# Performance work log

Measured on AMD Instinct MI355X. Metric: run time of the kernel, lower is better.

## Reference

```python
import jax, jax.numpy as jnp
import numpy as np

N, E, F_IN, D, EF, L, G = 50000, 800000, 92, 64, 50, 3, 128
EPS = 1e-5


def setup_inputs() -> dict:
    key = jax.random.key(0)
    ks = jax.random.split(key, 16)
    Z = 2 * D + EF  # concat dim for CGConv messages
    inp = {
        "x": jax.random.normal(ks[0], (N, F_IN), dtype=jnp.float32),
        "edge_index": jax.random.randint(ks[1], (2, E), 0, N, dtype=jnp.int32),
        "edge_attr": jax.random.uniform(ks[2], (E, EF), dtype=jnp.float32),
        "batch": jnp.sort(jax.random.randint(ks[3], (N,), 0, G, dtype=jnp.int32)),
        "pre_W": jax.random.normal(ks[4], (F_IN, D), dtype=jnp.float32) * 0.05,
        "pre_b": jnp.zeros((D,), jnp.float32),
        "Wf": jax.random.normal(ks[5], (L, Z, D), dtype=jnp.float32) * 0.05,
        "bf": jnp.zeros((L, D), jnp.float32),
        "Ws": jax.random.normal(ks[6], (L, Z, D), dtype=jnp.float32) * 0.05,
        "bs": jnp.zeros((L, D), jnp.float32),
        "bn_gamma": jnp.ones((L, D), jnp.float32) + 0.1 * jax.random.normal(ks[7], (L, D), dtype=jnp.float32),
        "bn_beta": 0.1 * jax.random.normal(ks[8], (L, D), dtype=jnp.float32),
        "bn_mean": 0.1 * jax.random.normal(ks[9], (L, D), dtype=jnp.float32),
        "bn_var": jax.random.uniform(ks[10], (L, D), dtype=jnp.float32, minval=0.5, maxval=1.5),
        "post_W": jax.random.normal(ks[11], (D, D), dtype=jnp.float32) * 0.05,
        "post_b": jnp.zeros((D,), jnp.float32),
        "out_W": jax.random.normal(ks[12], (D, 1), dtype=jnp.float32) * 0.05,
        "out_b": jnp.zeros((1,), jnp.float32),
    }
    return inp


def reference(x, edge_index, edge_attr, batch, pre_W, pre_b, Wf, bf, Ws, bs,
              bn_gamma, bn_beta, bn_mean, bn_var, post_W, post_b, out_W, out_b):
    src = edge_index[0]  # x_j (source)
    dst = edge_index[1]  # x_i (target, aggregation index)

    # pre FC + relu
    h = jax.nn.relu(x @ pre_W + pre_b)

    # in-degree for mean aggregation
    deg = jax.ops.segment_sum(jnp.ones((E,), h.dtype), dst, num_segments=N)
    deg = jnp.maximum(deg, 1.0)[:, None]

    for l in range(L):
        # CGConv: z_ij = [h_i || h_j || e_ij]
        z = jnp.concatenate([h[dst], h[src], edge_attr], axis=-1)  # [E, 2D+EF]
        m = jax.nn.sigmoid(z @ Wf[l] + bf[l]) * jax.nn.softplus(z @ Ws[l] + bs[l])
        agg = jax.ops.segment_sum(m, dst, num_segments=N) / deg
        h = h + agg  # residual in CGConv
        # BatchNorm1d (eval mode, running stats); dropout is identity in eval
        h = bn_gamma[l] * (h - bn_mean[l]) * jax.lax.rsqrt(bn_var[l] + EPS) + bn_beta[l]

    # early global_mean_pool over graphs
    cnt = jax.ops.segment_sum(jnp.ones((N,), h.dtype), batch, num_segments=G)
    cnt = jnp.maximum(cnt, 1.0)[:, None]
    g = jax.ops.segment_sum(h, batch, num_segments=G) / cnt  # [G, D]

    g = jax.nn.relu(g @ post_W + post_b)
    return g @ out_W + out_b  # [G, 1]
```

## Files before the change

### kernel.cpp

```cpp
#include <hip/hip_runtime.h>
#include <cmath>

#define N_NODES 50000
#define N_EDGES 800000
#define F_IN 92
#define DIM 64
#define EF 50
#define NLAYER 3
#define NGRAPH 128
#define ZROWS 178

__global__ __launch_bounds__(256, 3) void pre_fc(const float* __restrict__ x,
                                                 const float* __restrict__ W,
                                                 const float* __restrict__ b,
                                                 float* __restrict__ h, int N)
{
    const int lane = threadIdx.x & 63;
    const int wid  = blockIdx.x * (blockDim.x >> 6) + (threadIdx.x >> 6);
    const int nw   = gridDim.x * (blockDim.x >> 6);
    float w[F_IN];
#pragma unroll
    for (int k = 0; k < F_IN; ++k) w[k] = W[k * DIM + lane];
    const float bb = b[lane];
#pragma unroll 1
    for (int n = wid; n < N; n += nw) {
        const int nu = __builtin_amdgcn_readfirstlane(n);
        const float* xr = x + (size_t)nu * F_IN;
        float a = bb;
#pragma unroll
        for (int k = 0; k < F_IN; ++k) a = fmaf(xr[k], w[k], a);
        h[(size_t)nu * DIM + lane] = fmaxf(a, 0.f);
    }
}

__global__ __launch_bounds__(256) void hist_cnt(const int* __restrict__ ei, int E,
                                                const int* __restrict__ batch, int N,
                                                int* __restrict__ hist,
                                                float* __restrict__ cnt)
{
    const int i = blockIdx.x * blockDim.x + threadIdx.x;
    const int stride = gridDim.x * blockDim.x;
    for (int e = i; e < E; e += stride) atomicAdd(&hist[ei[E + e]], 1);
    for (int n = i; n < N; n += stride) unsafeAtomicAdd(&cnt[batch[n]], 1.f);
}

__global__ __launch_bounds__(256) void scan_offs(const int* __restrict__ hist,
                                                 int* __restrict__ offs, int Nn)
{
    __shared__ int ssum[256];
    const int t = threadIdx.x;
    const int seg = (Nn + 255) / 256;
    const int lo = t * seg;
    const int hi = (lo + seg < Nn) ? lo + seg : Nn;
    int s = 0;
    for (int i = lo; i < hi; ++i) s += hist[i];
    ssum[t] = s;
    __syncthreads();
    if (t == 0) {
        int run = 0;
        for (int i = 0; i < 256; ++i) { int v = ssum[i]; ssum[i] = run; run += v; }
        offs[Nn] = run;
    }
    __syncthreads();
    int run = ssum[t];
    for (int i = lo; i < hi; ++i) { offs[i] = run; run += hist[i]; }
}

__global__ __launch_bounds__(256) void scatter_edges(const int* __restrict__ ei,
                                                     const int* __restrict__ offs,
                                                     int* __restrict__ cursor,
                                                     int* __restrict__ s_src,
                                                     int* __restrict__ s_dst,
                                                     int* __restrict__ s_eid, int E)
{
    const int i = blockIdx.x * blockDim.x + threadIdx.x;
    const int stride = gridDim.x * blockDim.x;
    for (int e = i; e < E; e += stride) {
        const int d = ei[E + e];
        const int s = ei[e];
        const int pos = offs[d] + atomicAdd(&cursor[d], 1);
        s_src[pos] = s;
        s_dst[pos] = d;
        s_eid[pos] = e;
    }
}

__global__ __launch_bounds__(256, 2) void node_proj(const float* __restrict__ h,
                                                    const float* __restrict__ Wfl,
                                                    const float* __restrict__ Wsl,
                                                    const float* __restrict__ bf,
                                                    const float* __restrict__ bs,
                                                    float* __restrict__ Pd,
                                                    float* __restrict__ Ps, int N)
{
    const int lane = threadIdx.x & 63;
    const int wid  = blockIdx.x * (blockDim.x >> 6) + (threadIdx.x >> 6);
    const int nw   = gridDim.x * (blockDim.x >> 6);
    const int half = wid & 1;
    const float* wfb = Wfl + (half ? DIM * DIM : 0);
    const float* wsb = Wsl + (half ? DIM * DIM : 0);
    float wf[DIM], ws[DIM];
#pragma unroll
    for (int k = 0; k < DIM; ++k) { wf[k] = wfb[k * DIM + lane]; ws[k] = wsb[k * DIM + lane]; }
    const float b0 = half ? 0.f : bf[lane];
    const float b1 = half ? 0.f : bs[lane];
    float* P = half ? Ps : Pd;
#pragma unroll 1
    for (int n = (wid >> 1); n < N; n += (nw >> 1)) {
        const int nu = __builtin_amdgcn_readfirstlane(n);
        const float* hr = h + (size_t)nu * DIM;
        float a0 = b0, a1 = b1;
#pragma unroll
        for (int k = 0; k < DIM; ++k) {
            const float v = hr[k];
            a0 = fmaf(v, wf[k], a0);
            a1 = fmaf(v, ws[k], a1);
        }
        P[(size_t)nu * 128 + lane]      = a0;
        P[(size_t)nu * 128 + 64 + lane] = a1;
    }
}

#define EA_PAD 51
#define TP_PAD 129
__global__ __launch_bounds__(512) void edge_fused(const int* __restrict__ s_src,
                                                  const int* __restrict__ s_dst,
                                                  const int* __restrict__ s_eid,
                                                  const float* __restrict__ eattr,
                                                  const float* __restrict__ Pd,
                                                  const float* __restrict__ Ps,
                                                  const float* __restrict__ WfE,
                                                  const float* __restrict__ WsE,
                                                  float* __restrict__ agg, int E)
{
    __shared__ float ea_lds[64 * EA_PAD];
    __shared__ float out_lds[64 * TP_PAD];

    const int tid = threadIdx.x;
    const int e0  = blockIdx.x * 64;

    {
        const int* eid = s_eid + e0;
        for (int idx = tid; idx < 64 * EF; idx += 512) {
            const int e = idx / EF;
            const int k = idx - e * EF;
            ea_lds[e * EA_PAD + k] = eattr[(size_t)eid[e] * EF + k];
        }
    }
    __syncthreads();

    {
        const int e  = tid & 63;
        const int wv = __builtin_amdgcn_readfirstlane(tid >> 6);
        const float* Wbase = (wv < 4) ? WfE : WsE;
        const int c0 = (wv & 3) * 16;
        const int cb = ((wv < 4) ? 0 : 64) + c0;

        float acc[16];
#pragma unroll
        for (int j = 0; j < 16; ++j) acc[j] = 0.f;

        const float* ear = ea_lds + e * EA_PAD;
#pragma unroll 5
        for (int k = 0; k < EF; ++k) {
            const float eak = ear[k];
            const float* wr = Wbase + k * DIM + c0;
#pragma unroll
            for (int j = 0; j < 16; ++j) acc[j] = fmaf(eak, wr[j], acc[j]);
        }
        float* orow = out_lds + e * TP_PAD + cb;
#pragma unroll
        for (int j = 0; j < 16; ++j) orow[j] = acc[j];
    }
    __syncthreads();

    {
        const int lane = tid & 63;
        const int wv   = __builtin_amdgcn_readfirstlane(tid >> 6);
        const int base = e0 + wv * 8;

        int dcur = s_dst[base];
        const float* pdr = Pd + (size_t)dcur * 128;
        float pd0 = pdr[lane], pd1 = pdr[64 + lane];
        float acc = 0.f;
#pragma unroll
        for (int i = 0; i < 8; ++i) {
            const int el = wv * 8 + i;
            const int eg = base + i;
            const int dd = s_dst[eg];
            const int ss = s_src[eg];
            if (dd != dcur) {
                unsafeAtomicAdd(&agg[(size_t)dcur * DIM + lane], acc);
                acc = 0.f;
                dcur = dd;
                pdr = Pd + (size_t)dcur * 128;
                pd0 = pdr[lane]; pd1 = pdr[64 + lane];
            }
            const float* psr = Ps + (size_t)ss * 128;
            const float zf = out_lds[el * TP_PAD + lane]      + pd0 + psr[lane];
            const float zs = out_lds[el * TP_PAD + 64 + lane] + pd1 + psr[64 + lane];
            const float sig = 1.f / (1.f + __expf(-zf));
            const float sp  = fmaxf(zs, 0.f) + __logf(1.f + __expf(-fabsf(zs)));
            acc = fmaf(sig, sp, acc);
        }
        unsafeAtomicAdd(&agg[(size_t)dcur * DIM + lane], acc);
    }
}

__global__ __launch_bounds__(256) void node_update(float* __restrict__ h,
                                                   const float* __restrict__ agg,
                                                   const int* __restrict__ hist,
                                                   const float* __restrict__ gamma,
                                                   const float* __restrict__ beta,
                                                   const float* __restrict__ mean,
                                                   const float* __restrict__ var, int N)
{
    const int lane = threadIdx.x & 63;
    const float g  = gamma[lane];
    const float bt = beta[lane];
    const float mn = mean[lane];
    const float iv = rsqrtf(var[lane] + 1e-5f);
    const int idx = blockIdx.x * blockDim.x + threadIdx.x;
    const int stride = gridDim.x * blockDim.x;
    const int total = N * DIM;
    for (int i = idx; i < total; i += stride) {
        const int n = i >> 6;
        const float inv = 1.f / fmaxf((float)hist[n], 1.f);
        const float v = h[i] + agg[i] * inv;
        h[i] = fmaf(g, (v - mn) * iv, bt);
    }
}

__global__ __launch_bounds__(256) void pool_sum(const float* __restrict__ h,
                                                const int* __restrict__ batch,
                                                float* __restrict__ gsum, int N)
{
    const int lane = threadIdx.x & 63;
    const int wid  = blockIdx.x * (blockDim.x >> 6) + (threadIdx.x >> 6);
    const int nw   = gridDim.x * (blockDim.x >> 6);
    for (int n = wid; n < N; n += nw) {
        const int nu = __builtin_amdgcn_readfirstlane(n);
        const int b = batch[nu];
        unsafeAtomicAdd(&gsum[(size_t)b * DIM + lane], h[(size_t)nu * DIM + lane]);
    }
}

__global__ __launch_bounds__(64) void head(const float* __restrict__ gsum,
                                           const float* __restrict__ cnt,
                                           const float* __restrict__ postW,
                                           const float* __restrict__ postb,
                                           const float* __restrict__ outW,
                                           const float* __restrict__ outb,
                                           float* __restrict__ out)
{
    const int gi = blockIdx.x;
    const int lane = threadIdx.x;
    const float inv = 1.f / fmaxf(cnt[gi], 1.f);
    const float gval = gsum[(size_t)gi * DIM + lane] * inv;
    float acc = postb[lane];
#pragma unroll
    for (int k = 0; k < DIM; ++k) acc = fmaf(__shfl(gval, k, 64), postW[k * DIM + lane], acc);
    const float t = fmaxf(acc, 0.f);
    float prod = t * outW[lane];
#pragma unroll
    for (int off = 32; off > 0; off >>= 1) prod += __shfl_down(prod, off, 64);
    if (lane == 0) out[gi] = prod + outb[0];
}

extern "C" void kernel_launch(void* const* d_in, const int* in_sizes, int n_in,
                              void* d_out, int out_size, void* d_ws, size_t ws_size,
                              hipStream_t stream)
{
    const float* x     = (const float*)d_in[0];
    const int*   ei    = (const int*)d_in[1];
    const float* eattr = (const float*)d_in[2];
    const int*   batch = (const int*)d_in[3];
    const float* preW  = (const float*)d_in[4];
    const float* preb  = (const float*)d_in[5];
    const float* Wf    = (const float*)d_in[6];
    const float* bf    = (const float*)d_in[7];
    const float* Ws    = (const float*)d_in[8];
    const float* bs    = (const float*)d_in[9];
    const float* gamma = (const float*)d_in[10];
    const float* beta  = (const float*)d_in[11];
    const float* mean  = (const float*)d_in[12];
    const float* var   = (const float*)d_in[13];
    const float* postW = (const float*)d_in[14];
    const float* postb = (const float*)d_in[15];
    const float* outW  = (const float*)d_in[16];
    const float* outb  = (const float*)d_in[17];
    float* out = (float*)d_out;

    const int N = N_NODES, E = N_EDGES, G = NGRAPH;

    char* p = (char*)d_ws;
    float* h      = (float*)p; p += (size_t)N * DIM * 4;
    float* Pd     = (float*)p; p += (size_t)N * 128 * 4;
    float* Ps     = (float*)p; p += (size_t)N * 128 * 4;
    float* agg    = (float*)p; p += (size_t)N * DIM * 4;
    float* gsum   = (float*)p; p += (size_t)G * DIM * 4;
    float* cnt    = (float*)p; p += (size_t)G * 4;
    int*   hist   = (int*)p;   p += (size_t)N * 4;
    int*   cursor = (int*)p;   p += (size_t)N * 4;
    int*   offs   = (int*)p;   p += (size_t)(N + 1) * 4;
    int*   s_src  = (int*)p;   p += (size_t)E * 4;
    int*   s_dst  = (int*)p;   p += (size_t)E * 4;
    int*   s_eid  = (int*)p;   p += (size_t)E * 4;

    hipMemsetAsync(gsum, 0, ((size_t)G * DIM + G + N + N) * 4, stream);

    hist_cnt<<<512, 256, 0, stream>>>(ei, E, batch, N, hist, cnt);
    scan_offs<<<1, 256, 0, stream>>>(hist, offs, N);
    scatter_edges<<<512, 256, 0, stream>>>(ei, offs, cursor, s_src, s_dst, s_eid, E);

    pre_fc<<<512, 256, 0, stream>>>(x, preW, preb, h, N);

    for (int l = 0; l < NLAYER; ++l) {
        const float* Wfl = Wf + (size_t)l * ZROWS * DIM;
        const float* Wsl = Ws + (size_t)l * ZROWS * DIM;
        hipMemsetAsync(agg, 0, (size_t)N * DIM * 4, stream);
        node_proj<<<512, 256, 0, stream>>>(h, Wfl, Wsl, bf + l * DIM, bs + l * DIM, Pd, Ps, N);
        edge_fused<<<E / 64, 512, 0, stream>>>(s_src, s_dst, s_eid, eattr, Pd, Ps,
                                               Wfl + 2 * DIM * DIM, Wsl + 2 * DIM * DIM, agg, E);
        node_update<<<1024, 256, 0, stream>>>(h, agg, hist, gamma + l * DIM, beta + l * DIM,
                                              mean + l * DIM, var + l * DIM, N);
    }

    pool_sum<<<512, 256, 0, stream>>>(h, batch, gsum, N);
    head<<<G, 64, 0, stream>>>(gsum, cnt, postW, postb, outW, outb, out);
}
```

Measured before the change: 1.187 ms.

## Compute edge-attribute projection with split-bf16 MFMA instead of scalar FMAs

```diff
diff --git a/kernel.cpp b/kernel.cpp
--- a/kernel.cpp
+++ b/kernel.cpp
@@ -9,6 +9,17 @@
 #define NLAYER 3
 #define NGRAPH 128
 #define ZROWS 178
+
+using short8 = __attribute__((ext_vector_type(8))) short;
+using f32x4  = __attribute__((ext_vector_type(4))) float;
+
+__device__ __forceinline__ unsigned short f2bf(float v) {
+    unsigned int u = __float_as_uint(v);
+    return (unsigned short)((u + 0x7FFFu + ((u >> 16) & 1u)) >> 16);
+}
+__device__ __forceinline__ float bf2f(unsigned short h) {
+    return __uint_as_float(((unsigned int)h) << 16);
+}
 
 __global__ __launch_bounds__(256, 3) void pre_fc(const float* __restrict__ x,
                                                  const float* __restrict__ W,
@@ -85,6 +96,27 @@
     }
 }
 
+__global__ __launch_bounds__(256) void prep_wsplit(const float* __restrict__ Wf,
+                                                   const float* __restrict__ Ws,
+                                                   unsigned short* __restrict__ Wth,
+                                                   unsigned short* __restrict__ Wtl)
+{
+    const int i = blockIdx.x * blockDim.x + threadIdx.x;
+    if (i >= NLAYER * 128 * 64) return;
+    const int l = i >> 13;
+    const int rem = i & 8191;
+    const int c = rem >> 6;
+    const int k = rem & 63;
+    float v = 0.f;
+    if (k < EF) {
+        const size_t base = (size_t)l * ZROWS * DIM + (size_t)(2 * DIM + k) * DIM;
+        v = (c < 64) ? Wf[base + c] : Ws[base + (c - 64)];
+    }
+    const unsigned short hb = f2bf(v);
+    Wth[i] = hb;
+    Wtl[i] = f2bf(v - bf2f(hb));
+}
+
 __global__ __launch_bounds__(256, 2) void node_proj(const float* __restrict__ h,
                                                     const float* __restrict__ Wfl,
                                                     const float* __restrict__ Wsl,
@@ -121,7 +153,7 @@
     }
 }
 
-#define EA_PAD 51
+#define EA_STR 68
 #define TP_PAD 129
 __global__ __launch_bounds__(512) void edge_fused(const int* __restrict__ s_src,
                                                   const int* __restrict__ s_dst,
@@ -129,11 +161,11 @@
                                                   const float* __restrict__ eattr,
                                                   const float* __restrict__ Pd,
                                                   const float* __restrict__ Ps,
-                                                  const float* __restrict__ WfE,
-                                                  const float* __restrict__ WsE,
+                                                  const unsigned short* __restrict__ Wth,
+                                                  const unsigned short* __restrict__ Wtl,
                                                   float* __restrict__ agg, int E)
 {
-    __shared__ float ea_lds[64 * EA_PAD];
+    __shared__ float ea_lds[64 * EA_STR];
     __shared__ float out_lds[64 * TP_PAD];
 
     const int tid = threadIdx.x;
@@ -141,36 +173,65 @@
 
     {
         const int* eid = s_eid + e0;
-        for (int idx = tid; idx < 64 * EF; idx += 512) {
-            const int e = idx / EF;
-            const int k = idx - e * EF;
-            ea_lds[e * EA_PAD + k] = eattr[(size_t)eid[e] * EF + k];
+#pragma unroll
+        for (int it = 0; it < 8; ++it) {
+            const int idx = tid + it * 512;
+            const int e = idx >> 6;
+            const int k = idx & 63;
+            ea_lds[e * EA_STR + k] = (k < EF) ? eattr[(size_t)eid[e] * EF + k] : 0.f;
         }
     }
     __syncthreads();
 
     {
-        const int e  = tid & 63;
+        const int l  = tid & 63;
         const int wv = __builtin_amdgcn_readfirstlane(tid >> 6);
-        const float* Wbase = (wv < 4) ? WfE : WsE;
-        const int c0 = (wv & 3) * 16;
-        const int cb = ((wv < 4) ? 0 : 64) + c0;
-
-        float acc[16];
-#pragma unroll
-        for (int j = 0; j < 16; ++j) acc[j] = 0.f;
-
-        const float* ear = ea_lds + e * EA_PAD;
-#pragma unroll 5
-        for (int k = 0; k < EF; ++k) {
-            const float eak = ear[k];
-            const float* wr = Wbase + k * DIM + c0;
-#pragma unroll
-            for (int j = 0; j < 16; ++j) acc[j] = fmaf(eak, wr[j], acc[j]);
-        }
-        float* orow = out_lds + e * TP_PAD + cb;
-#pragma unroll
-        for (int j = 0; j < 16; ++j) orow[j] = acc[j];
+        const int mt = wv & 3;
+        const int ng = wv >> 2;
+        const int row = mt * 16 + (l & 15);
+        const int kq  = (l >> 4) * 8;
+
+        short8 ah[2], al[2];
+#pragma unroll
+        for (int kc = 0; kc < 2; ++kc) {
+            const float* ap = ea_lds + row * EA_STR + kc * 32 + kq;
+#pragma unroll
+            for (int j = 0; j < 8; ++j) {
+                const float v = ap[j];
+                const unsigned short hb = f2bf(v);
+                ah[kc][j] = (short)hb;
+                al[kc][j] = (short)f2bf(v - bf2f(hb));
+            }
+        }
+
+        f32x4 acc[4];
+#pragma unroll
+        for (int nt = 0; nt < 4; ++nt) acc[nt] = (f32x4){0.f, 0.f, 0.f, 0.f};
+
+#pragma unroll
+        for (int nt = 0; nt < 4; ++nt) {
+            const int col = ng * 64 + nt * 16 + (l & 15);
+            const unsigned short* bp = Wth + (size_t)col * 64 + kq;
+            const unsigned short* lp = Wtl + (size_t)col * 64 + kq;
+#pragma unroll
+            for (int kc = 0; kc < 2; ++kc) {
+                const short8 bh = *reinterpret_cast<const short8*>(bp + kc * 32);
+                const short8 bl = *reinterpret_cast<const short8*>(lp + kc * 32);
+                acc[nt] = __builtin_amdgcn_mfma_f32_16x16x32_bf16(ah[kc], bh, acc[nt], 0, 0, 0);
+                acc[nt] = __builtin_amdgcn_mfma_f32_16x16x32_bf16(ah[kc], bl, acc[nt], 0, 0, 0);
+                acc[nt] = __builtin_amdgcn_mfma_f32_16x16x32_bf16(al[kc], bh, acc[nt], 0, 0, 0);
+            }
+        }
+
+#pragma unroll
+        for (int nt = 0; nt < 4; ++nt) {
+            const int oc = ng * 64 + nt * 16 + (l & 15);
+#pragma unroll
+            for (int r = 0; r < 4; ++r) {
+                const int orow = mt * 16 + (l >> 4) * 4 + r;
+                out_lds[orow * TP_PAD + oc] = acc[nt][r];
+            }
+        }
     }
     __syncthreads();
 
@@ -306,12 +367,15 @@
     int*   s_src  = (int*)p;   p += (size_t)E * 4;
     int*   s_dst  = (int*)p;   p += (size_t)E * 4;
     int*   s_eid  = (int*)p;   p += (size_t)E * 4;
+    unsigned short* Wth = (unsigned short*)p; p += (size_t)NLAYER * 128 * 64 * 2;
+    unsigned short* Wtl = (unsigned short*)p; p += (size_t)NLAYER * 128 * 64 * 2;
 
     hipMemsetAsync(gsum, 0, ((size_t)G * DIM + G + N + N) * 4, stream);
 
     hist_cnt<<<512, 256, 0, stream>>>(ei, E, batch, N, hist, cnt);
     scan_offs<<<1, 256, 0, stream>>>(hist, offs, N);
     scatter_edges<<<512, 256, 0, stream>>>(ei, offs, cursor, s_src, s_dst, s_eid, E);
+    prep_wsplit<<<(NLAYER * 128 * 64 + 255) / 256, 256, 0, stream>>>(Wf, Ws, Wth, Wtl);
 
     pre_fc<<<512, 256, 0, stream>>>(x, preW, preb, h, N);
 
@@ -321,7 +385,8 @@
         hipMemsetAsync(agg, 0, (size_t)N * DIM * 4, stream);
         node_proj<<<512, 256, 0, stream>>>(h, Wfl, Wsl, bf + l * DIM, bs + l * DIM, Pd, Ps, N);
         edge_fused<<<E / 64, 512, 0, stream>>>(s_src, s_dst, s_eid, eattr, Pd, Ps,
-                                               Wfl + 2 * DIM * DIM, Wsl + 2 * DIM * DIM, agg, E);
+                                               Wth + (size_t)l * 8192, Wtl + (size_t)l * 8192,
+                                               agg, E);
         node_update<<<1024, 256, 0, stream>>>(h, agg, hist, gamma + l * DIM, beta + l * DIM,
                                               mean + l * DIM, var + l * DIM, N);
     }
```

Result: slower. 1.418 ms (+19.5%).
